# Kernel tuning notes

Hardware: AMD Instinct MI355X
Metric: run time of the kernel (lower is better)

The kernel has to match this reference:

```python
import math
import jax, jax.numpy as jnp
import numpy as np

# ---- module constants (from init_kwargs / SpectralBias.__init__) ----
B, H, L, DH = 1, 16, 2048, 64
M_MODES, K_FREQ = 2, 6
HIDDEN, OUT = max(128, 2 * DH), 4 * M_MODES + 1  # 128, 9 (use_slope=True)
L_TRAIN, L_MAX = 2048, 1_000_000
W_MIN = 2.0 * math.pi / L_MAX
W_MAX = 2.0 * math.pi / L_TRAIN
OMEGAS = np.logspace(math.log10(W_MIN), math.log10(W_MAX), K_FREQ).astype(np.float32)
DELTA_STAR_MAX = float(L_TRAIN - 1)
WIDTH_MIN, WIDTH_MAX = 32.0, 256.0
C_SCALE, TAU, EPS = 0.01, 64.0, 1e-9


def setup_inputs() -> dict:
    key = jax.random.key(0)
    k0, k1, k2 = jax.random.split(key, 3)
    q = jax.random.normal(k0, (B, H, L, DH), jnp.float32)
    w1 = jax.random.normal(k1, (HIDDEN, DH), jnp.float32) * (DH ** -0.5)
    b1 = jnp.zeros((HIDDEN,), jnp.float32)
    w2 = jax.random.normal(k2, (OUT, HIDDEN), jnp.float32) * 0.02
    # _init_outputs: first M output biases initialized to linspace(-6, -4, M)
    b2 = jnp.zeros((OUT,), jnp.float32).at[:M_MODES].set(jnp.linspace(-6.0, -4.0, M_MODES))
    return {"q": q, "w1": w1, "b1": b1, "w2": w2, "b2": b2}


def reference(q, w1, b1, w2, b2):
    """Query-conditioned Fourier relative-position bias b[b,h,i,j] for Delta = i - j >= 0.

    Per-query MLP emits, for each of M modes: gate logit, soft center delta*,
    width sigma, amplitude c, plus one slope term. Bias is a Fourier bump
    sum_k a_k(sigma) * cos(omega_k * (Delta - delta*)) with its Delta-mean
    subtracted (subtract_b0), scaled by sigmoid(gate) * c_scale * softplus(c),
    plus an ALiBi-like slope -softplus(s) * Delta / tau. Zero for Delta < 0.
    """
    omegas = jnp.asarray(OMEGAS)                       # [K]
    # shared-across-heads MLP (Linear -> SiLU -> Linear)
    y = jax.nn.silu(q @ w1.T + b1) @ w2.T + b2         # [B,H,L,4M+1]
    p = jax.nn.sigmoid(y[..., :M_MODES])               # gates          [B,H,L,M]
    dstar = jax.nn.sigmoid(y[..., M_MODES:2 * M_MODES]) * DELTA_STAR_MAX
    sigma = WIDTH_MIN + jax.nn.sigmoid(y[..., 2 * M_MODES:3 * M_MODES]) * (WIDTH_MAX - WIDTH_MIN)
    c = C_SCALE * jax.nn.softplus(y[..., 3 * M_MODES:4 * M_MODES])
    slope = jax.nn.softplus(y[..., 4 * M_MODES])       # [B,H,L]

    # Gaussian spectral weights per mode: a_k = exp(-0.5 * omega_k^2 * sigma^2)
    a = jnp.exp(-0.5 * (omegas ** 2) * (sigma[..., None] ** 2))   # [B,H,L,M,K]
    a = a / (a.sum(-1, keepdims=True) + EPS)
    phase = omegas * dstar[..., None]                              # [B,H,L,M,K]
    amp = (p * c)[..., None] * a
    # collapse modes into per-query cos/sin coefficients
    coefC = (amp * jnp.cos(phase)).sum(-2)             # [B,H,L,K]
    coefS = (amp * jnp.sin(phase)).sum(-2)

    d_arr = jnp.arange(L, dtype=jnp.float32)
    # subtract_b0: mean of the bump over Delta in [0, L)
    cos_mean = jnp.cos(omegas[:, None] * d_arr).mean(-1)           # [K]
    sin_mean = jnp.sin(omegas[:, None] * d_arr).mean(-1)
    b0 = coefC @ cos_mean + coefS @ sin_mean           # [B,H,L]

    delta = d_arr[:, None] - d_arr[None, :]            # [L,L], i - j
    mask = delta >= 0.0
    dp = jnp.where(mask, delta, 0.0)
    cos_d = jnp.cos(omegas[:, None, None] * dp)        # [K,L,L]
    sin_d = jnp.sin(omegas[:, None, None] * dp)
    fourier = jnp.einsum('bhik,kij->bhij', coefC, cos_d) + jnp.einsum('bhik,kij->bhij', coefS, sin_d)
    bias = fourier - b0[..., None] - (slope[..., None] / TAU) * dp
    return jnp.where(mask, bias, 0.0)                  # [B,H,L,L]
```

## Files before the change

### kernel.cpp

```cpp
#include <hip/hip_runtime.h>
#include <math.h>


struct BiasParams {
    float omg[6];
    float omg2[6];
    float cw[6];
    float sw[6];
};

__device__ __forceinline__ float sigmoidf_(float x) { return 1.0f / (1.0f + expf(-x)); }
__device__ __forceinline__ float softplusf_(float x) {
    return fmaxf(x, 0.0f) + log1pf(expf(-fabsf(x)));
}

__global__ void sb_mean_kernel(float* __restrict__ ws, BiasParams P)
{
    const int k    = threadIdx.x >> 6;
    const int lane = threadIdx.x & 63;
    const float om = P.omg[k];
    float cacc = 0.f, sacc = 0.f;
    for (int d = lane; d < 2048; d += 64) {
        float s, c;
        sincosf(om * (float)d, &s, &c);
        cacc += c; sacc += s;
    }
    #pragma unroll
    for (int off = 32; off >= 1; off >>= 1) {
        cacc += __shfl_down(cacc, off);
        sacc += __shfl_down(sacc, off);
    }
    if (lane == 0) {
        ws[k]     = cacc * (1.0f / 2048.0f);
        ws[6 + k] = sacc * (1.0f / 2048.0f);
    }
}

__global__ __launch_bounds__(256) void sb_coef_kernel(
    const float* __restrict__ q,  const float* __restrict__ w1,
    const float* __restrict__ b1, const float* __restrict__ w2,
    const float* __restrict__ b2, float* __restrict__ ws, BiasParams P)
{
    __shared__ __align__(16) float w1L[64 * 132];
    __shared__ __align__(16) float w2L[9 * 128];
    __shared__ __align__(16) float qs[64 * 65];

    const int t      = threadIdx.x;
    const int lane   = t & 63;
    const int w      = t >> 6;
    const int qblock = blockIdx.x << 6;

    for (int idx = t; idx < 128 * 64; idx += 256) {
        int h = idx >> 6, d = idx & 63;
        w1L[d * 132 + h] = w1[idx];
    }
    for (int idx = t; idx < 9 * 128; idx += 256) w2L[idx] = w2[idx];
    {
        const float* qg = q + ((size_t)qblock << 6);
        for (int idx = t; idx < 64 * 64; idx += 256)
            qs[(idx >> 6) * 65 + (idx & 63)] = qg[idx];
    }
    __syncthreads();

    const int h0 = w << 5;
    float acc[32];
    #pragma unroll
    for (int u = 0; u < 32; ++u) acc[u] = b1[h0 + u];

    for (int d = 0; d < 64; ++d) {
        float qv = qs[lane * 65 + d];
        const float4* wr = (const float4*)(&w1L[d * 132 + h0]);
        #pragma unroll
        for (int u4 = 0; u4 < 8; ++u4) {
            float4 wv = wr[u4];
            acc[u4 * 4 + 0] = fmaf(qv, wv.x, acc[u4 * 4 + 0]);
            acc[u4 * 4 + 1] = fmaf(qv, wv.y, acc[u4 * 4 + 1]);
            acc[u4 * 4 + 2] = fmaf(qv, wv.z, acc[u4 * 4 + 2]);
            acc[u4 * 4 + 3] = fmaf(qv, wv.w, acc[u4 * 4 + 3]);
        }
    }
    #pragma unroll
    for (int u = 0; u < 32; ++u) acc[u] = acc[u] * sigmoidf_(acc[u]);

    float part[9];
    #pragma unroll
    for (int o = 0; o < 9; ++o) part[o] = 0.f;
    #pragma unroll
    for (int o = 0; o < 9; ++o) {
        const float4* wr = (const float4*)(&w2L[o * 128 + h0]);
        #pragma unroll
        for (int u4 = 0; u4 < 8; ++u4) {
            float4 wv = wr[u4];
            part[o] = fmaf(acc[u4 * 4 + 0], wv.x, part[o]);
            part[o] = fmaf(acc[u4 * 4 + 1], wv.y, part[o]);
            part[o] = fmaf(acc[u4 * 4 + 2], wv.z, part[o]);
            part[o] = fmaf(acc[u4 * 4 + 3], wv.w, part[o]);
        }
    }
    __syncthreads();
    float* pl = qs;
    #pragma unroll
    for (int o = 0; o < 9; ++o) pl[t * 13 + o] = part[o];
    __syncthreads();

    if (w == 0) {
        float y[9];
        #pragma unroll
        for (int o = 0; o < 9; ++o)
            y[o] = b2[o] + pl[lane * 13 + o] + pl[(64 + lane) * 13 + o]
                 + pl[(128 + lane) * 13 + o] + pl[(192 + lane) * 13 + o];

        float C[6], S[6];
        #pragma unroll
        for (int k = 0; k < 6; ++k) { C[k] = 0.f; S[k] = 0.f; }
        float slope = softplusf_(y[8]);

        #pragma unroll
        for (int m = 0; m < 2; ++m) {
            float p   = sigmoidf_(y[m]);
            float dst = sigmoidf_(y[2 + m]) * 2047.0f;
            float sg  = 32.0f + sigmoidf_(y[4 + m]) * 224.0f;
            float cm  = 0.01f * softplusf_(y[6 + m]);
            float s2  = sg * sg;
            float a[6]; float asum = 0.f;
            #pragma unroll
            for (int k = 0; k < 6; ++k) { a[k] = expf(-0.5f * P.omg2[k] * s2); asum += a[k]; }
            float inv = 1.0f / (asum + 1e-9f);
            float pc  = p * cm;
            #pragma unroll
            for (int k = 0; k < 6; ++k) {
                float sn, cn;
                sincosf(P.omg[k] * dst, &sn, &cn);
                float amp = pc * (a[k] * inv);
                C[k] = fmaf(amp, cn, C[k]);
                S[k] = fmaf(amp, sn, S[k]);
            }
        }
        float b0 = 0.f;
        #pragma unroll
        for (int k = 0; k < 6; ++k) b0 += C[k] * ws[k] + S[k] * ws[6 + k];

        float* cf = ws + 16 + ((size_t)(qblock + lane) << 4);
        ((float4*)cf)[0] = make_float4(C[0], C[1], C[2], C[3]);
        ((float4*)cf)[1] = make_float4(C[4], C[5], S[0], S[1]);
        ((float4*)cf)[2] = make_float4(S[2], S[3], S[4], S[5]);
        ((float4*)cf)[3] = make_float4(b0, slope * (1.0f / 64.0f), 0.f, 0.f);
    }
}

__global__ __launch_bounds__(256) void sb_bias_kernel(
    const float* __restrict__ ws, float* __restrict__ out, BiasParams P)
{
    const int rid = blockIdx.x;
    const int i   = rid & 2047;
    const float* cf = ws + 16 + ((size_t)rid << 4);
    const float4 c0 = ((const float4*)cf)[0];
    const float4 c1 = ((const float4*)cf)[1];
    const float4 c2 = ((const float4*)cf)[2];
    const float4 c3 = ((const float4*)cf)[3];
    const float C[6] = {c0.x, c0.y, c0.z, c0.w, c1.x, c1.y};
    const float S[6] = {c1.z, c1.w, c2.x, c2.y, c2.z, c2.w};
    const float b0 = c3.x, slt = c3.y;

    const int j0 = threadIdx.x << 3;
    const int D0 = i - j0;
    float res[8];

    if (D0 < 0) {
        #pragma unroll
        for (int s = 0; s < 8; ++s) res[s] = 0.f;
    } else {
        float g[6], hh[6];
        #pragma unroll
        for (int k = 0; k < 6; ++k) {
            float sn, cn;
            __sincosf(P.omg[k] * (float)D0, &sn, &cn);
            g[k]  = fmaf(C[k], cn,  S[k] * sn);
            hh[k] = fmaf(S[k], cn, -C[k] * sn);
        }
        float dpf = (float)D0;
        #pragma unroll
        for (int s = 0; s < 8; ++s) {
            float four = ((g[0] + g[1]) + (g[2] + g[3])) + (g[4] + g[5]);
            res[s] = (s <= D0) ? (four - b0 - slt * dpf) : 0.f;
            #pragma unroll
            for (int k = 0; k < 6; ++k) {
                float gn = fmaf(g[k],  P.cw[k], -hh[k] * P.sw[k]);
                float hn = fmaf(hh[k], P.cw[k],  g[k]  * P.sw[k]);
                g[k] = gn; hh[k] = hn;
            }
            dpf -= 1.0f;
        }
    }
    float4* op = (float4*)(out + (((size_t)rid) << 11) + j0);
    op[0] = make_float4(res[0], res[1], res[2], res[3]);
    op[1] = make_float4(res[4], res[5], res[6], res[7]);
}

extern "C" void kernel_launch(void* const* d_in, const int* in_sizes, int n_in,
                              void* d_out, int out_size, void* d_ws, size_t ws_size,
                              hipStream_t stream) {
    const float* q  = (const float*)d_in[0];
    const float* w1 = (const float*)d_in[1];
    const float* b1 = (const float*)d_in[2];
    const float* w2 = (const float*)d_in[3];
    const float* b2 = (const float*)d_in[4];
    float* out = (float*)d_out;
    float* ws  = (float*)d_ws;

    BiasParams P;
    const double l0 = log10(2.0 * M_PI / 1.0e6);
    const double l1 = log10(2.0 * M_PI / 2048.0);
    for (int k = 0; k < 6; ++k) {
        double e  = l0 + (l1 - l0) * ((double)k / 5.0);
        float  wf = (float)pow(10.0, e);
        P.omg[k]  = wf;
        P.omg2[k] = wf * wf;
        P.cw[k]   = (float)cos((double)wf);
        P.sw[k]   = (float)sin((double)wf);
    }

    sb_mean_kernel<<<1, 384, 0, stream>>>(ws, P);
    sb_coef_kernel<<<512, 256, 0, stream>>>(q, w1, b1, w2, b2, ws, P);
    sb_bias_kernel<<<16 * 2048, 256, 0, stream>>>(ws, out, P);
}
```

Measured before the change: 308.8 us.

## Precompute Fourier means on host, rework MLP kernel, nontemporal stores in bias kernel

```diff
diff --git a/kernel.cpp b/kernel.cpp
--- a/kernel.cpp
+++ b/kernel.cpp
@@ -1,39 +1,21 @@
 #include <hip/hip_runtime.h>
 #include <math.h>
 
+
+typedef float f32x4_ __attribute__((ext_vector_type(4)));
 
 struct BiasParams {
     float omg[6];
     float omg2[6];
     float cw[6];
     float sw[6];
+    float cmn[6];
+    float smn[6];
 };
 
 __device__ __forceinline__ float sigmoidf_(float x) { return 1.0f / (1.0f + expf(-x)); }
 __device__ __forceinline__ float softplusf_(float x) {
     return fmaxf(x, 0.0f) + log1pf(expf(-fabsf(x)));
-}
-
-__global__ void sb_mean_kernel(float* __restrict__ ws, BiasParams P)
-{
-    const int k    = threadIdx.x >> 6;
-    const int lane = threadIdx.x & 63;
-    const float om = P.omg[k];
-    float cacc = 0.f, sacc = 0.f;
-    for (int d = lane; d < 2048; d += 64) {
-        float s, c;
-        sincosf(om * (float)d, &s, &c);
-        cacc += c; sacc += s;
-    }
-    #pragma unroll
-    for (int off = 32; off >= 1; off >>= 1) {
-        cacc += __shfl_down(cacc, off);
-        sacc += __shfl_down(sacc, off);
-    }
-    if (lane == 0) {
-        ws[k]     = cacc * (1.0f / 2048.0f);
-        ws[6 + k] = sacc * (1.0f / 2048.0f);
-    }
 }
 
 __global__ __launch_bounds__(256) void sb_coef_kernel(
@@ -41,64 +23,47 @@
     const float* __restrict__ b1, const float* __restrict__ w2,
     const float* __restrict__ b2, float* __restrict__ ws, BiasParams P)
 {
-    __shared__ __align__(16) float w1L[64 * 132];
-    __shared__ __align__(16) float w2L[9 * 128];
-    __shared__ __align__(16) float qs[64 * 65];
-
-    const int t      = threadIdx.x;
-    const int lane   = t & 63;
-    const int w      = t >> 6;
-    const int qblock = blockIdx.x << 6;
-
-    for (int idx = t; idx < 128 * 64; idx += 256) {
-        int h = idx >> 6, d = idx & 63;
-        w1L[d * 132 + h] = w1[idx];
-    }
-    for (int idx = t; idx < 9 * 128; idx += 256) w2L[idx] = w2[idx];
+    __shared__ float pl[256 * 13];
+    const int t    = threadIdx.x;
+    const int lane = t & 63;
+    const int w    = t >> 6;
+    const int qid  = (blockIdx.x << 6) + lane;
+
+    float qv[64];
     {
-        const float* qg = q + ((size_t)qblock << 6);
-        for (int idx = t; idx < 64 * 64; idx += 256)
-            qs[(idx >> 6) * 65 + (idx & 63)] = qg[idx];
-    }
-    __syncthreads();
-
-    const int h0 = w << 5;
-    float acc[32];
-    #pragma unroll
-    for (int u = 0; u < 32; ++u) acc[u] = b1[h0 + u];
-
-    for (int d = 0; d < 64; ++d) {
-        float qv = qs[lane * 65 + d];
-        const float4* wr = (const float4*)(&w1L[d * 132 + h0]);
-        #pragma unroll
-        for (int u4 = 0; u4 < 8; ++u4) {
-            float4 wv = wr[u4];
-            acc[u4 * 4 + 0] = fmaf(qv, wv.x, acc[u4 * 4 + 0]);
-            acc[u4 * 4 + 1] = fmaf(qv, wv.y, acc[u4 * 4 + 1]);
-            acc[u4 * 4 + 2] = fmaf(qv, wv.z, acc[u4 * 4 + 2]);
-            acc[u4 * 4 + 3] = fmaf(qv, wv.w, acc[u4 * 4 + 3]);
-        }
-    }
-    #pragma unroll
-    for (int u = 0; u < 32; ++u) acc[u] = acc[u] * sigmoidf_(acc[u]);
+        const float4* qr = (const float4*)(q + ((size_t)qid << 6));
+        #pragma unroll
+        for (int j = 0; j < 16; ++j) {
+            float4 v = qr[j];
+            qv[4*j+0] = v.x; qv[4*j+1] = v.y; qv[4*j+2] = v.z; qv[4*j+3] = v.w;
+        }
+    }
+
+    const int h0 = __builtin_amdgcn_readfirstlane(w << 5);
+    const float* __restrict__ w1u = w1 + (size_t)h0 * 64;
 
     float part[9];
     #pragma unroll
     for (int o = 0; o < 9; ++o) part[o] = 0.f;
-    #pragma unroll
-    for (int o = 0; o < 9; ++o) {
-        const float4* wr = (const float4*)(&w2L[o * 128 + h0]);
-        #pragma unroll
-        for (int u4 = 0; u4 < 8; ++u4) {
-            float4 wv = wr[u4];
-            part[o] = fmaf(acc[u4 * 4 + 0], wv.x, part[o]);
-            part[o] = fmaf(acc[u4 * 4 + 1], wv.y, part[o]);
-            part[o] = fmaf(acc[u4 * 4 + 2], wv.z, part[o]);
-            part[o] = fmaf(acc[u4 * 4 + 3], wv.w, part[o]);
-        }
-    }
-    __syncthreads();
-    float* pl = qs;
+
+    #pragma unroll 4
+    for (int h = 0; h < 32; ++h) {
+        const float* __restrict__ wr = w1u + h * 64;
+        float a0 = 0.f, a1 = 0.f, a2 = 0.f, a3 = 0.f;
+        #pragma unroll
+        for (int d = 0; d < 64; d += 4) {
+            a0 = fmaf(qv[d+0], wr[d+0], a0);
+            a1 = fmaf(qv[d+1], wr[d+1], a1);
+            a2 = fmaf(qv[d+2], wr[d+2], a2);
+            a3 = fmaf(qv[d+3], wr[d+3], a3);
+        }
+        float a = ((a0 + a1) + (a2 + a3)) + b1[h0 + h];
+        a = a * sigmoidf_(a);
+        #pragma unroll
+        for (int o = 0; o < 9; ++o)
+            part[o] = fmaf(a, w2[o * 128 + h0 + h], part[o]);
+    }
+
     #pragma unroll
     for (int o = 0; o < 9; ++o) pl[t * 13 + o] = part[o];
     __syncthreads();
@@ -138,9 +103,9 @@
         }
         float b0 = 0.f;
         #pragma unroll
-        for (int k = 0; k < 6; ++k) b0 += C[k] * ws[k] + S[k] * ws[6 + k];
-
-        float* cf = ws + 16 + ((size_t)(qblock + lane) << 4);
+        for (int k = 0; k < 6; ++k) b0 += C[k] * P.cmn[k] + S[k] * P.smn[k];
+
+        float* cf = ws + ((size_t)qid << 4);
         ((float4*)cf)[0] = make_float4(C[0], C[1], C[2], C[3]);
         ((float4*)cf)[1] = make_float4(C[4], C[5], S[0], S[1]);
         ((float4*)cf)[2] = make_float4(S[2], S[3], S[4], S[5]);
@@ -153,7 +118,7 @@
 {
     const int rid = blockIdx.x;
     const int i   = rid & 2047;
-    const float* cf = ws + 16 + ((size_t)rid << 4);
+    const float* cf = ws + ((size_t)rid << 4);
     const float4 c0 = ((const float4*)cf)[0];
     const float4 c1 = ((const float4*)cf)[1];
     const float4 c2 = ((const float4*)cf)[2];
@@ -178,23 +143,39 @@
             g[k]  = fmaf(C[k], cn,  S[k] * sn);
             hh[k] = fmaf(S[k], cn, -C[k] * sn);
         }
-        float dpf = (float)D0;
-        #pragma unroll
-        for (int s = 0; s < 8; ++s) {
-            float four = ((g[0] + g[1]) + (g[2] + g[3])) + (g[4] + g[5]);
-            res[s] = (s <= D0) ? (four - b0 - slt * dpf) : 0.f;
-            #pragma unroll
-            for (int k = 0; k < 6; ++k) {
-                float gn = fmaf(g[k],  P.cw[k], -hh[k] * P.sw[k]);
-                float hn = fmaf(hh[k], P.cw[k],  g[k]  * P.sw[k]);
-                g[k] = gn; hh[k] = hn;
+        float e = fmaf(-slt, (float)D0, -b0);
+        if (D0 >= 7) {
+            #pragma unroll
+            for (int s = 0; s < 8; ++s) {
+                res[s] = (((g[0] + g[1]) + (g[2] + g[3])) + (g[4] + g[5])) + e;
+                e += slt;
+                #pragma unroll
+                for (int k = 0; k < 6; ++k) {
+                    float gn = fmaf(g[k],  P.cw[k], -hh[k] * P.sw[k]);
+                    float hn = fmaf(hh[k], P.cw[k],  g[k]  * P.sw[k]);
+                    g[k] = gn; hh[k] = hn;
+                }
             }
-            dpf -= 1.0f;
-        }
-    }
-    float4* op = (float4*)(out + (((size_t)rid) << 11) + j0);
-    op[0] = make_float4(res[0], res[1], res[2], res[3]);
-    op[1] = make_float4(res[4], res[5], res[6], res[7]);
+        } else {
+            #pragma unroll
+            for (int s = 0; s < 8; ++s) {
+                float four = ((g[0] + g[1]) + (g[2] + g[3])) + (g[4] + g[5]);
+                res[s] = (s <= D0) ? (four + e) : 0.f;
+                e += slt;
+                #pragma unroll
+                for (int k = 0; k < 6; ++k) {
+                    float gn = fmaf(g[k],  P.cw[k], -hh[k] * P.sw[k]);
+                    float hn = fmaf(hh[k], P.cw[k],  g[k]  * P.sw[k]);
+                    g[k] = gn; hh[k] = hn;
+                }
+            }
+        }
+    }
+    f32x4_* op = (f32x4_*)(out + (((size_t)rid) << 11) + j0);
+    f32x4_ v0 = {res[0], res[1], res[2], res[3]};
+    f32x4_ v1 = {res[4], res[5], res[6], res[7]};
+    __builtin_nontemporal_store(v0, op + 0);
+    __builtin_nontemporal_store(v1, op + 1);
 }
 
 extern "C" void kernel_launch(void* const* d_in, const int* in_sizes, int n_in,
@@ -218,9 +199,12 @@
         P.omg2[k] = wf * wf;
         P.cw[k]   = (float)cos((double)wf);
         P.sw[k]   = (float)sin((double)wf);
-    }
-
-    sb_mean_kernel<<<1, 384, 0, stream>>>(ws, P);
+        double cm = 0.0, sm = 0.0;
+        for (int d = 0; d < 2048; ++d) { cm += cos((double)wf * d); sm += sin((double)wf * d); }
+        P.cmn[k] = (float)(cm / 2048.0);
+        P.smn[k] = (float)(sm / 2048.0);
+    }
+
     sb_coef_kernel<<<512, 256, 0, stream>>>(q, w1, b1, w2, b2, ws, P);
     sb_bias_kernel<<<16 * 2048, 256, 0, stream>>>(ws, out, P);
 }
```

Measured after the change: 386.0 us. 1.25x slower.
